# Kernel optimization log

Hardware: AMD Instinct MI355X
Metric: run time of the kernel (lower is better)

Reference implementation:

```python
import jax, jax.numpy as jnp
import numpy as np

KER = 3          # CausalPool1d kernel
PAD_VAL = 1e-8   # left-pad value
K = 3            # harmonic_num
H = 4200         # rows of integral matrix
F = 321          # frequency bins


def setup_inputs() -> dict:
    key = jax.random.key(0)
    k1, k2, k3 = jax.random.split(key, 3)
    mag = jax.random.uniform(k1, (8, 2, F, 1000), dtype=jnp.float32)          # B,C,F,T (magnitude >= 0)
    integral_m = jax.random.normal(k2, (H, F), dtype=jnp.float32)             # buffer integral_m (squeezed)
    harmonic_loc = jax.random.normal(k3, (H, F), dtype=jnp.float32)           # buffer harmonic_loc (squeezed)
    return {"mag": mag, "integral_m": integral_m, "harmonic_loc": harmonic_loc, "freq_dim": F}


def reference(mag, integral_m, harmonic_loc, freq_dim):
    # harmonic_nominee: (B,C,H,T) = integral_m @ mag
    nominee = jnp.einsum('hf,bcft->bcht', integral_m, mag)
    # topk over the H axis (torch dim=-2); lax.top_k works on last axis -> move H last
    _, pos = jax.lax.top_k(jnp.moveaxis(nominee, 2, -1), K)  # (B,C,T,K), descending like torch
    pos = jnp.moveaxis(pos, -1, 2).astype(jnp.float32)       # (B,C,K,T)
    # CausalPool1d: left-pad (KER-1) with 1e-8, avg over window KER, stride 1 (vectorized over K)
    xp = jnp.pad(pos, ((0, 0), (0, 0), (0, 0), (KER - 1, 0)), constant_values=PAD_VAL)
    T = pos.shape[-1]
    choose = ((xp[..., 0:T] + xp[..., 1:T + 1] + xp[..., 2:T + 2]) / KER).astype(jnp.int32)  # (B,C,K,T)
    # gather harmonic_loc rows and accumulate over the K harmonics
    gathered = harmonic_loc[choose]          # (B,C,K,T,F)
    summed = gathered.sum(axis=2)            # (B,C,T,F)
    # (B,C,F,T) threshold mask, matching torch's (x > 0).float()
    out = (jnp.swapaxes(summed, -1, -2) > 0).astype(jnp.float32)
    return out
```

## Files before the change

kernel.cpp:

```cpp
#include <hip/hip_runtime.h>
#include <math.h>

#define F_DIM 321
#define H_DIM 4200
#define T_DIM 1000
#define NBC   16
#define KTOP  3
#define PADV  1e-8f

#define BM 32
#define BN 256
#define BK 16
#define NRT 132
#define NKT 20
#define NTT 4

typedef float v4f __attribute__((ext_vector_type(4)));
typedef __attribute__((address_space(3))) uint32_t lds_u32;
typedef const __attribute__((address_space(1))) uint32_t glb_u32;

__device__ __forceinline__ void ins3(float v, int i,
                                     float& v0, float& v1, float& v2,
                                     int& i0, int& i1, int& i2) {
  if (v > v0)      { v2 = v1; i2 = i1; v1 = v0; i1 = i0; v0 = v; i0 = i; }
  else if (v > v1) { v2 = v1; i2 = i1; v1 = v;  i1 = i; }
  else if (v > v2) { v2 = v;  i2 = i; }
}

__global__ __launch_bounds__(256)
void hi_k1_gemm_top3(const float* __restrict__ mag,
                     const float* __restrict__ im,
                     float* __restrict__ wv, int* __restrict__ wi,
                     int nsplit) {
  const int tid  = threadIdx.x;
  const int lane = tid & 63;
  const int w    = tid >> 6;
  const int t0 = blockIdx.x * BN;
  const int bc = blockIdx.y;
  const int sp = blockIdx.z;
  const int rt_begin = (sp * NRT) / nsplit;
  const int rt_end   = ((sp + 1) * NRT) / nsplit;

  __shared__ __align__(16) float Bs[2][BK * BN];
  float* mv = (float*)&Bs[0][0];
  int*   mi = (int*)(&Bs[0][0] + 4 * BN * KTOP);

  const float* magbc = mag + (size_t)bc * F_DIM * T_DIM;

  auto stageB = [&](int buf, int k0) {
#pragma unroll
    for (int i = 0; i < 4; ++i) {
      int kr = w * 4 + i;
      const float* src = magbc + (size_t)(k0 + kr) * T_DIM + t0 + lane * 4;
      __builtin_amdgcn_global_load_lds(
          (glb_u32*)src, (lds_u32*)&Bs[buf][kr * BN], 16, 0, 0);
    }
  };

  float gv0 = -INFINITY, gv1 = -INFINITY, gv2 = -INFINITY;
  int   gi0 = 0, gi1 = 0, gi2 = 0;

  for (int rt = rt_begin; rt < rt_end; ++rt) {
    const int h0 = rt * BM;
    int ab[8];
#pragma unroll
    for (int r = 0; r < 8; ++r) {
      int gh = h0 + w * 8 + r;
      if (gh >= H_DIM) gh = H_DIM - 1;
      ab[r] = __builtin_amdgcn_readfirstlane(gh * F_DIM);
    }

    float acc[8][4];
#pragma unroll
    for (int r = 0; r < 8; ++r)
#pragma unroll
      for (int c = 0; c < 4; ++c) acc[r][c] = 0.f;

    stageB(0, 0);
    stageB(1, BK);
    asm volatile("s_waitcnt vmcnt(4)" ::: "memory");
    __builtin_amdgcn_s_barrier();
    __builtin_amdgcn_sched_barrier(0);

    int cur = 0;
    for (int kt = 0; kt < NKT; ++kt) {
      const int k0 = kt * BK;
#pragma unroll 2
      for (int g = 0; g < 4; ++g) {
        const int kk0 = k0 + g * 4;
        float a[8][4];
#pragma unroll
        for (int r = 0; r < 8; ++r)
#pragma unroll
          for (int q = 0; q < 4; ++q)
            a[r][q] = im[ab[r] + kk0 + q];
        v4f Bv[4];
#pragma unroll
        for (int q = 0; q < 4; ++q)
          Bv[q] = *(const v4f*)(&Bs[cur][(g * 4 + q) * BN + lane * 4]);
#pragma unroll
        for (int r = 0; r < 8; ++r)
#pragma unroll
          for (int q = 0; q < 4; ++q)
#pragma unroll
            for (int c = 0; c < 4; ++c)
              acc[r][c] = fmaf(a[r][q], Bv[q][c], acc[r][c]);
      }

      asm volatile("" ::: "memory");
      __builtin_amdgcn_s_barrier();
      __builtin_amdgcn_sched_barrier(0);

      if (kt + 2 < NKT) {
        stageB(cur, (kt + 2) * BK);
        asm volatile("s_waitcnt vmcnt(4)" ::: "memory");
      } else {
        asm volatile("s_waitcnt vmcnt(0)" ::: "memory");
      }
      asm volatile("" ::: "memory");
      __builtin_amdgcn_s_barrier();
      __builtin_amdgcn_sched_barrier(0);
      cur ^= 1;
    }

    {
      float bt[4];
#pragma unroll
      for (int c = 0; c < 4; ++c) {
        int gt = t0 + lane * 4 + c;
        bt[c] = (gt < T_DIM) ? magbc[(size_t)(F_DIM - 1) * T_DIM + gt] : 0.f;
      }
#pragma unroll
      for (int r = 0; r < 8; ++r) {
        float av = im[ab[r] + (F_DIM - 1)];
#pragma unroll
        for (int c = 0; c < 4; ++c) acc[r][c] = fmaf(av, bt[c], acc[r][c]);
      }
    }

#pragma unroll
    for (int c = 0; c < 4; ++c) {
      const int col = lane * 4 + c;
      float v0 = -INFINITY, v1 = -INFINITY, v2 = -INFINITY;
      int   i0 = 0, i1 = 0, i2 = 0;
#pragma unroll
      for (int r = 0; r < 8; ++r) {
        int gh = h0 + w * 8 + r;
        float v = (gh < H_DIM) ? acc[r][c] : -INFINITY;
        ins3(v, gh, v0, v1, v2, i0, i1, i2);
      }
      mv[(w * BN + col) * 3 + 0] = v0;
      mv[(w * BN + col) * 3 + 1] = v1;
      mv[(w * BN + col) * 3 + 2] = v2;
      mi[(w * BN + col) * 3 + 0] = i0;
      mi[(w * BN + col) * 3 + 1] = i1;
      mi[(w * BN + col) * 3 + 2] = i2;
    }
    __syncthreads();
    {
      const int col = tid;
#pragma unroll
      for (int ww = 0; ww < 4; ++ww)
#pragma unroll
        for (int j = 0; j < 3; ++j) {
          float v = mv[(ww * BN + col) * 3 + j];
          int   i = mi[(ww * BN + col) * 3 + j];
          ins3(v, i, gv0, gv1, gv2, gi0, gi1, gi2);
        }
    }
    __syncthreads();
  }

  {
    int t = t0 + tid;
    if (t < T_DIM) {
      size_t base = ((size_t)(bc * nsplit + sp) * KTOP) * T_DIM + t;
      wv[base]             = gv0;
      wv[base + T_DIM]     = gv1;
      wv[base + 2 * T_DIM] = gv2;
      wi[base]             = gi0;
      wi[base + T_DIM]     = gi1;
      wi[base + 2 * T_DIM] = gi2;
    }
  }
}

__global__ __launch_bounds__(256, 4)
void hi_k3_pool_gather(const float* __restrict__ wv, const int* __restrict__ wi,
                       const float* __restrict__ hl, float* __restrict__ out,
                       int nsplit) {
  const int tid = threadIdx.x;
  const int t0 = blockIdx.x * 64;
  const int bc = blockIdx.y;

  __shared__ float pos_lds[66 * KTOP];
  __shared__ int   rows[64 * KTOP];
  __shared__ float S[64 * 65];

  if (tid < 66) {
    int t = t0 - 2 + tid;
    float p0 = PADV, p1 = PADV, p2 = PADV;
    if (t >= 0 && t < T_DIM) {
      float v0 = -INFINITY, v1 = -INFINITY, v2 = -INFINITY;
      int i0 = 0, i1 = 0, i2 = 0;
      for (int sp = 0; sp < nsplit; ++sp)
        for (int j = 0; j < KTOP; ++j) {
          size_t idx = ((size_t)(bc * nsplit + sp) * KTOP + j) * T_DIM + t;
          ins3(wv[idx], wi[idx], v0, v1, v2, i0, i1, i2);
        }
      p0 = (float)i0; p1 = (float)i1; p2 = (float)i2;
    }
    pos_lds[tid * KTOP + 0] = p0;
    pos_lds[tid * KTOP + 1] = p1;
    pos_lds[tid * KTOP + 2] = p2;
  }
  __syncthreads();
  if (tid < 64) {
#pragma unroll
    for (int k = 0; k < KTOP; ++k) {
      float s = (pos_lds[tid * KTOP + k] + pos_lds[(tid + 1) * KTOP + k])
                + pos_lds[(tid + 2) * KTOP + k];
      rows[tid * KTOP + k] = (int)(s / 3.0f);
    }
  }
  __syncthreads();

  const int w = tid >> 6, lane = tid & 63;
  for (int fc = 0; fc < 6; ++fc) {
    const int f0 = fc * 64;
    for (int i = 0; i < 16; ++i) {
      int tl = w * 16 + i;
      int r0 = rows[tl * KTOP + 0];
      int r1 = rows[tl * KTOP + 1];
      int r2 = rows[tl * KTOP + 2];
      int f = f0 + lane;
      float s = 0.f;
      if (f < F_DIM)
        s = (hl[(size_t)r0 * F_DIM + f] + hl[(size_t)r1 * F_DIM + f])
            + hl[(size_t)r2 * F_DIM + f];
      S[tl * 65 + lane] = s;
    }
    __syncthreads();
#pragma unroll
    for (int i = 0; i < 16; ++i) {
      int e = tid + 256 * i;
      int fl = e >> 6, tl = e & 63;
      int f = f0 + fl, t = t0 + tl;
      if (f < F_DIM && t < T_DIM)
        out[((size_t)bc * F_DIM + f) * T_DIM + t] = (S[tl * 65 + fl] > 0.f) ? 1.f : 0.f;
    }
    __syncthreads();
  }
}

extern "C" void kernel_launch(void* const* d_in, const int* in_sizes, int n_in,
                              void* d_out, int out_size, void* d_ws, size_t ws_size,
                              hipStream_t stream) {
  const float* mag = (const float*)d_in[0];
  const float* im  = (const float*)d_in[1];
  const float* hl  = (const float*)d_in[2];
  float* out = (float*)d_out;

  int nsplit = 8;
  if (ws_size >= (size_t)NBC * 32 * KTOP * T_DIM * 8) nsplit = 32;
  else if (ws_size >= (size_t)NBC * 16 * KTOP * T_DIM * 8) nsplit = 16;
  float* wv = (float*)d_ws;
  int*   wi = (int*)d_ws + (size_t)NBC * nsplit * KTOP * T_DIM;

  dim3 g1(NTT, NBC, nsplit);
  hipLaunchKernelGGL(hi_k1_gemm_top3, g1, dim3(256), 0, stream, mag, im, wv, wi, nsplit);

  dim3 g3((T_DIM + 63) / 64, NBC);
  hipLaunchKernelGGL(hi_k3_pool_gather, g3, dim3(256), 0, stream, wv, wi, hl, out, nsplit);
}
```

Before: 960.3 us.

## Load GEMM B operand directly to registers with double buffering instead of LDS

The magnitude tiles used in the GEMM+top-3 kernel are no longer staged through double-buffered LDS with async global-to-LDS loads. Each lane now loads its four v4f columns straight from global memory into registers, alternating two register sets so the next group's loads overlap the current group's FMAs. This removes the per-k-tile barriers and LDS reads. In exchange, all four waves in a block fetch the same B data redundantly through the cache, and register pressure rises.

```diff
diff --git a/kernel.cpp b/kernel.cpp
--- a/kernel.cpp
+++ b/kernel.cpp
@@ -10,14 +10,11 @@
 
 #define BM 32
 #define BN 256
-#define BK 16
 #define NRT 132
-#define NKT 20
+#define NG  80
 #define NTT 4
 
 typedef float v4f __attribute__((ext_vector_type(4)));
-typedef __attribute__((address_space(3))) uint32_t lds_u32;
-typedef const __attribute__((address_space(1))) uint32_t glb_u32;
 
 __device__ __forceinline__ void ins3(float v, int i,
                                      float& v0, float& v1, float& v2,
@@ -26,6 +23,28 @@
   else if (v > v1) { v2 = v1; i2 = i1; v1 = v;  i1 = i; }
   else if (v > v2) { v2 = v;  i2 = i; }
 }
+
+#define LOADB(B0, B1, B2, B3, g) do {                                  \
+    const float* _p = pB + (size_t)((g) * 4) * T_DIM;                  \
+    B0 = *(const v4f*)(_p);                                            \
+    B1 = *(const v4f*)(_p + T_DIM);                                    \
+    B2 = *(const v4f*)(_p + 2 * T_DIM);                                \
+    B3 = *(const v4f*)(_p + 3 * T_DIM);                                \
+  } while (0)
+
+#define FMAG(B0, B1, B2, B3, g) do {                                   \
+    float _a[8][4];                                                    \
+    _Pragma("unroll") for (int r = 0; r < 8; ++r)                      \
+      _Pragma("unroll") for (int q = 0; q < 4; ++q)                    \
+        _a[r][q] = im[ab[r] + (g) * 4 + q];                            \
+    _Pragma("unroll") for (int r = 0; r < 8; ++r)                      \
+      _Pragma("unroll") for (int c = 0; c < 4; ++c) {                  \
+        acc[r][c] = fmaf(_a[r][0], B0[c], acc[r][c]);                  \
+        acc[r][c] = fmaf(_a[r][1], B1[c], acc[r][c]);                  \
+        acc[r][c] = fmaf(_a[r][2], B2[c], acc[r][c]);                  \
+        acc[r][c] = fmaf(_a[r][3], B3[c], acc[r][c]);                  \
+      }                                                                \
+  } while (0)
 
 __global__ __launch_bounds__(256)
 void hi_k1_gemm_top3(const float* __restrict__ mag,
@@ -41,21 +60,11 @@
   const int rt_begin = (sp * NRT) / nsplit;
   const int rt_end   = ((sp + 1) * NRT) / nsplit;
 
-  __shared__ __align__(16) float Bs[2][BK * BN];
-  float* mv = (float*)&Bs[0][0];
-  int*   mi = (int*)(&Bs[0][0] + 4 * BN * KTOP);
+  __shared__ float mv[4 * BN * KTOP];
+  __shared__ int   mi[4 * BN * KTOP];
 
   const float* magbc = mag + (size_t)bc * F_DIM * T_DIM;
-
-  auto stageB = [&](int buf, int k0) {
-#pragma unroll
-    for (int i = 0; i < 4; ++i) {
-      int kr = w * 4 + i;
-      const float* src = magbc + (size_t)(k0 + kr) * T_DIM + t0 + lane * 4;
-      __builtin_amdgcn_global_load_lds(
-          (glb_u32*)src, (lds_u32*)&Bs[buf][kr * BN], 16, 0, 0);
-    }
-  };
+  const float* pB = magbc + t0 + lane * 4;
 
   float gv0 = -INFINITY, gv1 = -INFINITY, gv2 = -INFINITY;
   int   gi0 = 0, gi1 = 0, gi2 = 0;
@@ -76,51 +85,16 @@
 #pragma unroll
       for (int c = 0; c < 4; ++c) acc[r][c] = 0.f;
 
-    stageB(0, 0);
-    stageB(1, BK);
-    asm volatile("s_waitcnt vmcnt(4)" ::: "memory");
-    __builtin_amdgcn_s_barrier();
-    __builtin_amdgcn_sched_barrier(0);
-
-    int cur = 0;
-    for (int kt = 0; kt < NKT; ++kt) {
-      const int k0 = kt * BK;
-#pragma unroll 2
-      for (int g = 0; g < 4; ++g) {
-        const int kk0 = k0 + g * 4;
-        float a[8][4];
-#pragma unroll
-        for (int r = 0; r < 8; ++r)
-#pragma unroll
-          for (int q = 0; q < 4; ++q)
-            a[r][q] = im[ab[r] + kk0 + q];
-        v4f Bv[4];
-#pragma unroll
-        for (int q = 0; q < 4; ++q)
-          Bv[q] = *(const v4f*)(&Bs[cur][(g * 4 + q) * BN + lane * 4]);
-#pragma unroll
-        for (int r = 0; r < 8; ++r)
-#pragma unroll
-          for (int q = 0; q < 4; ++q)
-#pragma unroll
-            for (int c = 0; c < 4; ++c)
-              acc[r][c] = fmaf(a[r][q], Bv[q][c], acc[r][c]);
-      }
-
-      asm volatile("" ::: "memory");
-      __builtin_amdgcn_s_barrier();
-      __builtin_amdgcn_sched_barrier(0);
-
-      if (kt + 2 < NKT) {
-        stageB(cur, (kt + 2) * BK);
-        asm volatile("s_waitcnt vmcnt(4)" ::: "memory");
-      } else {
-        asm volatile("s_waitcnt vmcnt(0)" ::: "memory");
-      }
-      asm volatile("" ::: "memory");
-      __builtin_amdgcn_s_barrier();
-      __builtin_amdgcn_sched_barrier(0);
-      cur ^= 1;
+    v4f Bc0, Bc1, Bc2, Bc3, Bn0, Bn1, Bn2, Bn3;
+    LOADB(Bc0, Bc1, Bc2, Bc3, 0);
+
+#pragma unroll 1
+    for (int gs = 0; gs < NG / 2; ++gs) {
+      const int ge = 2 * gs, go = 2 * gs + 1;
+      LOADB(Bn0, Bn1, Bn2, Bn3, go);
+      FMAG(Bc0, Bc1, Bc2, Bc3, ge);
+      if (ge + 2 < NG) LOADB(Bc0, Bc1, Bc2, Bc3, ge + 2);
+      FMAG(Bn0, Bn1, Bn2, Bn3, go);
     }
 
     {
```

Measured after the change: 938.1 us. 1.02x faster.
